# Optimization experiments

Measured on AMD Instinct MI355X. Metric: run time of the kernel, lower is better.

## Reference

```python
import jax, jax.numpy as jnp
import numpy as np

TAU = 0.07          # contrastive temperature
GAMMA = 2.0         # focal gamma
W_FOCAL = 0.6
W_CONTRASTIVE = 0.2
IGNORE_INDEX = -100
MAX_ANCHORS = 8     # hardcoded cap in ContrastiveLoss
N_NEG_BATCHES = 4   # hardcoded other_batches[:4]


def setup_inputs() -> dict:
    key = jax.random.key(0)
    ks = jax.random.split(key, 5)
    B, M, V = 64, 128, 5003
    S, D = 200, 128
    return {
        "masked_logits": jax.random.normal(ks[0], (B, M, V), dtype=jnp.float32),
        "masked_targets": jax.random.randint(ks[1], (B, M), 0, V, dtype=jnp.int32),
        "masked_mask": jax.random.randint(ks[2], (B, M), 0, 2, dtype=jnp.int32),
        "product_embeddings": jax.random.normal(ks[3], (B, S, D), dtype=jnp.float32),
        "product_ids": jax.random.randint(ks[4], (B, S), 0, V, dtype=jnp.int32),
        "attention_mask": jnp.ones((B, S), dtype=jnp.int32),
    }


def focal_loss(logits, targets, mask):
    # logits [B,M,V] -> flatten to [B*M,V] as in torch
    B, M, V = logits.shape
    logits = logits.reshape(B * M, V)
    targets = targets.reshape(-1)
    mask = mask.reshape(-1)
    valid = (targets != IGNORE_INDEX) & (mask == 1)
    t = jnp.clip(targets, 0, None)
    logp = jax.nn.log_softmax(logits, axis=-1)
    lp = jnp.take_along_axis(logp, t[:, None], axis=1)[:, 0]  # log p_t
    pt = jnp.exp(lp)
    fl = ((1.0 - pt) ** GAMMA) * (-lp) * valid.astype(logits.dtype)
    denom = valid.sum()
    return jnp.where(denom > 0, fl.sum() / denom.astype(logits.dtype), jnp.zeros((), logits.dtype))


def contrastive_loss(emb, pids, amask):
    # emb [B,S,D]
    B, S, D = emb.shape
    norm = jnp.maximum(jnp.linalg.norm(emb, axis=-1, keepdims=True), 1e-12)
    e = emb / norm  # F.normalize
    valid = (amask == 1) & (pids > 0)  # [B,S]
    # first 4 other batch indices per b (static, matches other_batches[:4])
    others = np.stack([np.array([i for i in range(B) if i != b][:N_NEG_BATCHES]) for b in range(B)])  # [B,4]

    def per_b(eb, vb, ne, nv):
        # eb [S,D], vb [S] bool, ne [4,S,D] neighbor embeddings, nv [4,S] their validity
        n = vb.sum()
        n_anch = jnp.minimum(n // 2, MAX_ANCHORS)
        # valid positions first (in order), padded with S
        pos_sorted = jnp.sort(jnp.where(vb, jnp.arange(S), S))
        a_idx = jnp.clip(pos_sorted[:MAX_ANCHORS], 0, S - 1)
        p_idx = jnp.clip(jnp.take(pos_sorted, n_anch + jnp.arange(MAX_ANCHORS), mode="clip"), 0, S - 1)
        sel = jnp.arange(MAX_ANCHORS) < n_anch  # active anchors
        a_e = eb[a_idx]  # [8,D]
        p_e = eb[p_idx]  # [8,D]
        pos_sim = (a_e * p_e).sum(-1) / TAU  # [8]
        negs = ne.reshape(-1, D)             # [4S,D]
        nvm = nv.reshape(-1)                 # [4S]
        neg_sim = (a_e @ negs.T) / TAU       # [8,4S]
        neg_sim = jnp.where(nvm[None, :], neg_sim, -1e9)
        lse = jax.nn.logsumexp(jnp.concatenate([pos_sim[:, None], neg_sim], axis=-1), axis=-1)
        loss_b = jnp.where(sel, lse - pos_sim, 0.0).sum()
        return loss_b, n_anch

    ne = e[others]       # [B,4,S,D]
    nv = valid[others]   # [B,4,S]
    losses, n_anch = jax.vmap(per_b)(e, valid, ne, nv)
    pairs = n_anch.sum()
    return jnp.where(pairs > 0, losses.sum() / pairs.astype(e.dtype), jnp.zeros((), e.dtype))


def reference(masked_logits, masked_targets, masked_mask, product_embeddings, product_ids, attention_mask):
    focal = focal_loss(masked_logits, masked_targets, masked_mask)
    contrastive = contrastive_loss(product_embeddings, product_ids, attention_mask)
    total = W_FOCAL * focal + W_CONTRASTIVE * contrastive
    return total
```

## Files before the change

kernel.cpp:

```cpp
#include <hip/hip_runtime.h>

#define V 5003
#define BB 64
#define SS 200
#define DD 128
#define TAU 0.07f
#define LOG2E 1.4426950408889634f
#define LN2 0.6931471805599453f
#define SHIFT 8.0f

#define WS_FS 0
#define WS_VC 2048
#define WS_CS 4096
#define WS_PR 4160

__global__ __launch_bounds__(256) void fused_loss_kernel(
    const float* __restrict__ logits,
    const int*   __restrict__ targets,
    const int*   __restrict__ mmask,
    const float* __restrict__ emb,
    const int*   __restrict__ pids,
    const int*   __restrict__ amask,
    float* __restrict__ ws)
{
    const int tid  = threadIdx.x;
    const int lane = tid & 63;
    const int wave = tid >> 6;

    __shared__ float fl_sh[4];
    __shared__ int   vc_sh[4];
    __shared__ __align__(16) float anchors[8][DD];
    __shared__ float possim[8];
    __shared__ unsigned char validb[SS];
    __shared__ short poslist[16];
    __shared__ int   n_sh;
    __shared__ int   nanch_sh;
    __shared__ float red[4][8];
    __shared__ float contrib_sh[8];

    if (blockIdx.x < 2048) {
        const int r = blockIdx.x * 4 + wave;
        const float* row = logits + (size_t)r * V;

        const int p = (4 - ((r * 3) & 3)) & 3;
        const int t = 3 - p;

        const float4* row4 = (const float4*)(row + p);
        const float C = -SHIFT * LOG2E;

        float s0 = 0.f, s1 = 0.f, s2 = 0.f, s3 = 0.f;

        int i = lane;
        #pragma unroll 4
        for (int it = 0; it < 19; ++it, i += 64) {
            float4 x = row4[i];
            s0 += exp2f(fmaf(x.x, LOG2E, C));
            s1 += exp2f(fmaf(x.y, LOG2E, C));
            s2 += exp2f(fmaf(x.z, LOG2E, C));
            s3 += exp2f(fmaf(x.w, LOG2E, C));
        }
        if (i < 1250) {
            float4 x = row4[i];
            s0 += exp2f(fmaf(x.x, LOG2E, C));
            s1 += exp2f(fmaf(x.y, LOG2E, C));
            s2 += exp2f(fmaf(x.z, LOG2E, C));
            s3 += exp2f(fmaf(x.w, LOG2E, C));
        }
        if (lane < p)
            s0 += exp2f(fmaf(row[lane], LOG2E, C));
        if (lane < t)
            s0 += exp2f(fmaf(row[p + 5000 + lane], LOG2E, C));

        float s = (s0 + s1) + (s2 + s3);
        for (int off = 32; off; off >>= 1)
            s += __shfl_xor(s, off, 64);

        if (lane == 0) {
            int tg  = targets[r];
            int mk  = mmask[r];
            bool valid = (tg != -100) && (mk == 1);
            int tc = tg < 0 ? 0 : tg;
            float xt  = row[tc];
            float lse = SHIFT + log2f(s) * LN2;
            float lp  = xt - lse;
            float pt  = exp2f(lp * LOG2E);
            float om  = 1.0f - pt;
            fl_sh[wave] = valid ? (om * om * (-lp)) : 0.0f;
            vc_sh[wave] = valid ? 1 : 0;
        }
        __syncthreads();
        if (tid == 0) {
            float fs = fl_sh[0] + fl_sh[1] + fl_sh[2] + fl_sh[3];
            int   vc = vc_sh[0] + vc_sh[1] + vc_sh[2] + vc_sh[3];
            ws[WS_FS + blockIdx.x] = fs;
            ws[WS_VC + blockIdx.x] = (float)vc;
        }
    } else {
        const int b = blockIdx.x - 2048;

        if (tid == 0) n_sh = 0;
        __syncthreads();

        if (tid < SS) {
            int idx = b * SS + tid;
            bool v = (amask[idx] == 1) && (pids[idx] > 0);
            validb[tid] = v ? 1 : 0;
            if (v) atomicAdd(&n_sh, 1);
        }
        __syncthreads();

        if (tid == 0) {
            int cnt = 0;
            for (int s = 0; s < SS && cnt < 16; ++s)
                if (validb[s]) poslist[cnt++] = (short)s;
            for (; cnt < 16; ++cnt) poslist[cnt] = (short)(SS - 1);
            int n  = n_sh;
            int na = n / 2;
            if (na > 8) na = 8;
            nanch_sh = na;
        }
        __syncthreads();
        const int n_anch = nanch_sh;

        const float2* embb = (const float2*)(emb + (size_t)b * SS * DD);
        for (int jj = 0; jj < 2; ++jj) {
            int j = wave + jj * 4;
            if (j < n_anch) {
                int ai = poslist[j];
                int pi = poslist[n_anch + j];
                float2 a2 = embb[ai * 64 + lane];
                float2 p2 = embb[pi * 64 + lane];
                float na_ = a2.x * a2.x + a2.y * a2.y;
                float np_ = p2.x * p2.x + p2.y * p2.y;
                float dp  = a2.x * p2.x + a2.y * p2.y;
                for (int off = 32; off; off >>= 1) {
                    na_ += __shfl_xor(na_, off, 64);
                    np_ += __shfl_xor(np_, off, 64);
                    dp  += __shfl_xor(dp,  off, 64);
                }
                float rna = 1.0f / fmaxf(sqrtf(na_), 1e-12f);
                float rnp = 1.0f / fmaxf(sqrtf(np_), 1e-12f);
                anchors[j][2 * lane]     = a2.x * rna;
                anchors[j][2 * lane + 1] = a2.y * rna;
                if (lane == 0) possim[j] = dp * rna * rnp * (1.0f / TAU);
            } else {
                anchors[j][2 * lane]     = 0.0f;
                anchors[j][2 * lane + 1] = 0.0f;
                if (lane == 0) possim[j] = 0.0f;
            }
        }
        __syncthreads();

        float part[8];
        #pragma unroll
        for (int j = 0; j < 8; ++j) part[j] = 0.0f;

        for (int i = 0; i < 4; ++i) {
            int g = tid + i * 256;
            if (g < 4 * SS) {
                int ol = g / SS;
                int s  = g - ol * SS;
                int o  = (ol >= b) ? ol + 1 : ol;
                int idx = o * SS + s;
                if (amask[idx] == 1 && pids[idx] > 0) {
                    const float4* nb = (const float4*)(emb + (size_t)idx * DD);
                    float acc[8];
                    float n2 = 0.0f;
                    #pragma unroll
                    for (int j = 0; j < 8; ++j) acc[j] = 0.0f;
                    #pragma unroll 8
                    for (int c = 0; c < DD / 4; ++c) {
                        float4 x = nb[c];
                        n2 += x.x * x.x + x.y * x.y + x.z * x.z + x.w * x.w;
                        #pragma unroll
                        for (int j = 0; j < 8; ++j) {
                            float4 a = ((const float4*)anchors[j])[c];
                            acc[j] += a.x * x.x + a.y * x.y + a.z * x.z + a.w * x.w;
                        }
                    }
                    float rn = 1.0f / fmaxf(sqrtf(n2), 1e-12f);
                    #pragma unroll
                    for (int j = 0; j < 8; ++j) {
                        float sim = acc[j] * rn * (1.0f / TAU);
                        part[j] += exp2f(sim * LOG2E);
                    }
                }
            }
        }

        #pragma unroll
        for (int j = 0; j < 8; ++j)
            for (int off = 32; off; off >>= 1)
                part[j] += __shfl_xor(part[j], off, 64);
        if (lane == 0) {
            #pragma unroll
            for (int j = 0; j < 8; ++j) red[wave][j] = part[j];
        }
        __syncthreads();

        if (tid < 8) {
            int j = tid;
            float ps = possim[j];
            float S  = exp2f(ps * LOG2E) + red[0][j] + red[1][j] + red[2][j] + red[3][j];
            float lse = log2f(S) * LN2;
            contrib_sh[j] = (j < n_anch) ? (lse - ps) : 0.0f;
        }
        __syncthreads();
        if (tid == 0) {
            float lb = 0.0f;
            for (int j = 0; j < 8; ++j) lb += contrib_sh[j];
            ws[WS_CS + b] = lb;
            ws[WS_PR + b] = (float)n_anch;
        }
    }
}

__global__ __launch_bounds__(256) void finalize_kernel(
    const float* __restrict__ ws, float* __restrict__ out)
{
    const int tid  = threadIdx.x;
    const int lane = tid & 63;
    const int wave = tid >> 6;
    __shared__ float r_fs[4], r_vc[4], r_cs[4], r_pr[4];

    float fs = 0.f, vc = 0.f, cs = 0.f, pr = 0.f;
    #pragma unroll
    for (int i = 0; i < 8; ++i) {
        fs += ws[WS_FS + tid + i * 256];
        vc += ws[WS_VC + tid + i * 256];
    }
    if (tid < 64) {
        cs = ws[WS_CS + tid];
        pr = ws[WS_PR + tid];
    }
    for (int off = 32; off; off >>= 1) {
        fs += __shfl_xor(fs, off, 64);
        vc += __shfl_xor(vc, off, 64);
        cs += __shfl_xor(cs, off, 64);
        pr += __shfl_xor(pr, off, 64);
    }
    if (lane == 0) { r_fs[wave] = fs; r_vc[wave] = vc; r_cs[wave] = cs; r_pr[wave] = pr; }
    __syncthreads();
    if (tid == 0) {
        float FS = r_fs[0] + r_fs[1] + r_fs[2] + r_fs[3];
        float VC = r_vc[0] + r_vc[1] + r_vc[2] + r_vc[3];
        float CS = r_cs[0] + r_cs[1] + r_cs[2] + r_cs[3];
        float PR = r_pr[0] + r_pr[1] + r_pr[2] + r_pr[3];
        float focal = VC > 0.0f ? FS / VC : 0.0f;
        float contr = PR > 0.0f ? CS / PR : 0.0f;
        out[0] = 0.6f * focal + 0.2f * contr;
    }
}

extern "C" void kernel_launch(void* const* d_in, const int* in_sizes, int n_in,
                              void* d_out, int out_size, void* d_ws, size_t ws_size,
                              hipStream_t stream) {
    const float* logits  = (const float*)d_in[0];
    const int*   targets = (const int*)d_in[1];
    const int*   mmask   = (const int*)d_in[2];
    const float* emb     = (const float*)d_in[3];
    const int*   pids    = (const int*)d_in[4];
    const int*   amask   = (const int*)d_in[5];
    float* out = (float*)d_out;
    float* ws  = (float*)d_ws;

    hipLaunchKernelGGL(fused_loss_kernel, dim3(2048 + 64), dim3(256), 0, stream,
                       logits, targets, mmask, emb, pids, amask, ws);
    hipLaunchKernelGGL(finalize_kernel, dim3(1), dim3(256), 0, stream, ws, out);
}
```

Baseline: 279.5 us.

## Assign one 256-thread block per logits row with all loads issued upfront

Each focal-loss row is now processed by a whole 256-thread block instead of one wave, so each thread issues five float4 loads at once rather than looping 19+ times per lane. The target logit and mask are loaded early, and per-row results go to workspace as float2 pairs. The finalize kernel widens to 1024 threads to reduce the 8192 row results. This aims to raise memory-level parallelism on a bandwidth-bound pass, at the cost of four times more blocks and an extra block-wide barrier per row.

```diff
diff --git a/kernel.cpp b/kernel.cpp
--- a/kernel.cpp
+++ b/kernel.cpp
@@ -9,10 +9,8 @@
 #define LN2 0.6931471805599453f
 #define SHIFT 8.0f
 
-#define WS_FS 0
-#define WS_VC 2048
-#define WS_CS 4096
-#define WS_PR 4160
+#define WS_CS 16384
+#define WS_PR 16448
 
 __global__ __launch_bounds__(256) void fused_loss_kernel(
     const float* __restrict__ logits,
@@ -27,8 +25,7 @@
     const int lane = tid & 63;
     const int wave = tid >> 6;
 
-    __shared__ float fl_sh[4];
-    __shared__ int   vc_sh[4];
+    __shared__ float wsum[4];
     __shared__ __align__(16) float anchors[8][DD];
     __shared__ float possim[8];
     __shared__ unsigned char validb[SS];
@@ -38,65 +35,63 @@
     __shared__ float red[4][8];
     __shared__ float contrib_sh[8];
 
-    if (blockIdx.x < 2048) {
-        const int r = blockIdx.x * 4 + wave;
+    if (blockIdx.x < 8192) {
+        const int r = blockIdx.x;
         const float* row = logits + (size_t)r * V;
+
+        const int tg = targets[r];
+        const int mk = mmask[r];
+        const int tc = tg < 0 ? 0 : tg;
+        const float xt = row[tc];
 
         const int p = (4 - ((r * 3) & 3)) & 3;
         const int t = 3 - p;
-
         const float4* row4 = (const float4*)(row + p);
         const float C = -SHIFT * LOG2E;
 
-        float s0 = 0.f, s1 = 0.f, s2 = 0.f, s3 = 0.f;
-
-        int i = lane;
-        #pragma unroll 4
-        for (int it = 0; it < 19; ++it, i += 64) {
-            float4 x = row4[i];
-            s0 += exp2f(fmaf(x.x, LOG2E, C));
-            s1 += exp2f(fmaf(x.y, LOG2E, C));
-            s2 += exp2f(fmaf(x.z, LOG2E, C));
-            s3 += exp2f(fmaf(x.w, LOG2E, C));
-        }
-        if (i < 1250) {
-            float4 x = row4[i];
-            s0 += exp2f(fmaf(x.x, LOG2E, C));
-            s1 += exp2f(fmaf(x.y, LOG2E, C));
-            s2 += exp2f(fmaf(x.z, LOG2E, C));
-            s3 += exp2f(fmaf(x.w, LOG2E, C));
-        }
-        if (lane < p)
-            s0 += exp2f(fmaf(row[lane], LOG2E, C));
-        if (lane < t)
-            s0 += exp2f(fmaf(row[p + 5000 + lane], LOG2E, C));
+        float4 v0 = row4[tid];
+        float4 v1 = row4[tid + 256];
+        float4 v2 = row4[tid + 512];
+        float4 v3 = row4[tid + 768];
+        const int  i4 = tid + 1024;
+        const bool ok = i4 < 1250;
+        float4 v4 = row4[ok ? i4 : 0];
+        float h = (tid < p) ? row[tid] : -1e30f;
+        float u = (tid < t) ? row[p + 5000 + tid] : -1e30f;
+        if (!ok) { v4.x = -1e30f; v4.y = -1e30f; v4.z = -1e30f; v4.w = -1e30f; }
+
+        float s0 = exp2f(fmaf(v0.x, LOG2E, C)) + exp2f(fmaf(v1.x, LOG2E, C))
+                 + exp2f(fmaf(v2.x, LOG2E, C)) + exp2f(fmaf(v3.x, LOG2E, C))
+                 + exp2f(fmaf(v4.x, LOG2E, C));
+        float s1 = exp2f(fmaf(v0.y, LOG2E, C)) + exp2f(fmaf(v1.y, LOG2E, C))
+                 + exp2f(fmaf(v2.y, LOG2E, C)) + exp2f(fmaf(v3.y, LOG2E, C))
+                 + exp2f(fmaf(v4.y, LOG2E, C));
+        float s2 = exp2f(fmaf(v0.z, LOG2E, C)) + exp2f(fmaf(v1.z, LOG2E, C))
+                 + exp2f(fmaf(v2.z, LOG2E, C)) + exp2f(fmaf(v3.z, LOG2E, C))
+                 + exp2f(fmaf(v4.z, LOG2E, C));
+        float s3 = exp2f(fmaf(v0.w, LOG2E, C)) + exp2f(fmaf(v1.w, LOG2E, C))
+                 + exp2f(fmaf(v2.w, LOG2E, C)) + exp2f(fmaf(v3.w, LOG2E, C))
+                 + exp2f(fmaf(v4.w, LOG2E, C));
+        s0 += exp2f(fmaf(h, LOG2E, C)) + exp2f(fmaf(u, LOG2E, C));
 
         float s = (s0 + s1) + (s2 + s3);
         for (int off = 32; off; off >>= 1)
             s += __shfl_xor(s, off, 64);
-
-        if (lane == 0) {
-            int tg  = targets[r];
-            int mk  = mmask[r];
+        if (lane == 0) wsum[wave] = s;
+        __syncthreads();
+
+        if (tid == 0) {
+            float S = (wsum[0] + wsum[1]) + (wsum[2] + wsum[3]);
             bool valid = (tg != -100) && (mk == 1);
-            int tc = tg < 0 ? 0 : tg;
-            float xt  = row[tc];
-            float lse = SHIFT + log2f(s) * LN2;
+            float lse = SHIFT + log2f(S) * LN2;
             float lp  = xt - lse;
             float pt  = exp2f(lp * LOG2E);
             float om  = 1.0f - pt;
-            fl_sh[wave] = valid ? (om * om * (-lp)) : 0.0f;
-            vc_sh[wave] = valid ? 1 : 0;
-        }
-        __syncthreads();
-        if (tid == 0) {
-            float fs = fl_sh[0] + fl_sh[1] + fl_sh[2] + fl_sh[3];
-            int   vc = vc_sh[0] + vc_sh[1] + vc_sh[2] + vc_sh[3];
-            ws[WS_FS + blockIdx.x] = fs;
-            ws[WS_VC + blockIdx.x] = (float)vc;
+            float fs  = valid ? (om * om * (-lp)) : 0.0f;
+            ((float2*)ws)[r] = make_float2(fs, valid ? 1.0f : 0.0f);
         }
     } else {
-        const int b = blockIdx.x - 2048;
+        const int b = blockIdx.x - 8192;
 
         if (tid == 0) n_sh = 0;
         __syncthreads();
@@ -215,19 +210,20 @@
     }
 }
 
-__global__ __launch_bounds__(256) void finalize_kernel(
+__global__ __launch_bounds__(1024) void finalize_kernel(
     const float* __restrict__ ws, float* __restrict__ out)
 {
     const int tid  = threadIdx.x;
     const int lane = tid & 63;
     const int wave = tid >> 6;
-    __shared__ float r_fs[4], r_vc[4], r_cs[4], r_pr[4];
-
+    __shared__ float r_fs[16], r_vc[16], r_cs[16], r_pr[16];
+
+    const float2* f2 = (const float2*)ws;
     float fs = 0.f, vc = 0.f, cs = 0.f, pr = 0.f;
     #pragma unroll
     for (int i = 0; i < 8; ++i) {
-        fs += ws[WS_FS + tid + i * 256];
-        vc += ws[WS_VC + tid + i * 256];
+        float2 v = f2[tid + i * 1024];
+        fs += v.x; vc += v.y;
     }
     if (tid < 64) {
         cs = ws[WS_CS + tid];
@@ -242,10 +238,9 @@
     if (lane == 0) { r_fs[wave] = fs; r_vc[wave] = vc; r_cs[wave] = cs; r_pr[wave] = pr; }
     __syncthreads();
     if (tid == 0) {
-        float FS = r_fs[0] + r_fs[1] + r_fs[2] + r_fs[3];
-        float VC = r_vc[0] + r_vc[1] + r_vc[2] + r_vc[3];
-        float CS = r_cs[0] + r_cs[1] + r_cs[2] + r_cs[3];
-        float PR = r_pr[0] + r_pr[1] + r_pr[2] + r_pr[3];
+        float FS = 0.f, VC = 0.f;
+        for (int w = 0; w < 16; ++w) { FS += r_fs[w]; VC += r_vc[w]; }
+        float CS = r_cs[0], PR = r_pr[0];
         float focal = VC > 0.0f ? FS / VC : 0.0f;
         float contr = PR > 0.0f ? CS / PR : 0.0f;
         out[0] = 0.6f * focal + 0.2f * contr;
@@ -264,7 +259,7 @@
     float* out = (float*)d_out;
     float* ws  = (float*)d_ws;
 
-    hipLaunchKernelGGL(fused_loss_kernel, dim3(2048 + 64), dim3(256), 0, stream,
+    hipLaunchKernelGGL(fused_loss_kernel, dim3(8192 + 64), dim3(256), 0, stream,
                        logits, targets, mmask, emb, pids, amask, ws);
-    hipLaunchKernelGGL(finalize_kernel, dim3(1), dim3(256), 0, stream, ws, out);
+    hipLaunchKernelGGL(finalize_kernel, dim3(1), dim3(1024), 0, stream, ws, out);
 }
```

New measurement: 281.6 us. Within noise of the previous version (+0.7%).
